# Performance work log

Measured on AMD Instinct MI355X. Metric: run time of the kernel, lower is better.

The kernel has to match this reference:

```python
import jax, jax.numpy as jnp
import numpy as np

N = 20000
E = 320000
IN_C, HID, OUT_C = 128, 64, 32
H12, H3 = 4, 1  # heads for conv1/conv2 and conv3
NEG_SLOPE = 0.2


def _glorot(key, shape):
    fan_in, fan_out = shape[0], shape[-1]
    lim = (6.0 / (fan_in + fan_out)) ** 0.5
    return jax.random.uniform(key, shape, jnp.float32, -lim, lim)


def setup_inputs() -> dict:
    key = jax.random.key(0)
    ks = jax.random.split(key, 16)
    x = jax.random.normal(ks[0], (N, IN_C), jnp.float32)
    edge_index = jax.random.randint(ks[1], (2, E), 0, N, jnp.int64)
    p = {
        'W1': _glorot(ks[2], (IN_C, H12 * HID)),
        'as1': _glorot(ks[3], (H12, HID)), 'ad1': _glorot(ks[4], (H12, HID)),
        'b1': jnp.zeros((HID,), jnp.float32),
        'W2': _glorot(ks[5], (HID, H12 * HID)),
        'as2': _glorot(ks[6], (H12, HID)), 'ad2': _glorot(ks[7], (H12, HID)),
        'b2': jnp.zeros((HID,), jnp.float32),
        'W3': _glorot(ks[8], (HID, H3 * OUT_C)),
        'as3': _glorot(ks[9], (H3, OUT_C)), 'ad3': _glorot(ks[10], (H3, OUT_C)),
        'b3': jnp.zeros((OUT_C,), jnp.float32),
        'Wm': _glorot(ks[11], (OUT_C, OUT_C)), 'bm': jnp.zeros((OUT_C,), jnp.float32),
        'Wv': _glorot(ks[12], (OUT_C, OUT_C)), 'bv': jnp.zeros((OUT_C,), jnp.float32),
    }
    return dict(x=x, edge_index=edge_index, **p)


def gat_layer(x, src, dst, W, a_src, a_dst, b, heads, out_c):
    # x: [N, in_c] -> h: [N, H, C]
    h = (x @ W).reshape(-1, heads, out_c)
    alpha_s = jnp.einsum('nhc,hc->nh', h, a_src)  # [N,H]
    alpha_d = jnp.einsum('nhc,hc->nh', h, a_dst)
    e = jax.nn.leaky_relu(alpha_s[src] + alpha_d[dst], NEG_SLOPE)  # [E',H]
    # segment softmax over incoming edges of each dst node
    m = jax.ops.segment_max(e, dst, num_segments=N)
    p = jnp.exp(e - m[dst])
    s = jax.ops.segment_sum(p, dst, num_segments=N)
    alpha = p / (s[dst] + 1e-16)  # [E',H]
    msg = h[src] * alpha[:, :, None]  # [E',H,C]
    out = jax.ops.segment_sum(msg, dst, num_segments=N)  # [N,H,C]
    return out.mean(axis=1) + b  # concat=False -> mean over heads


def reference(x, edge_index, W1, as1, ad1, b1, W2, as2, ad2, b2,
              W3, as3, ad3, b3, Wm, bm, Wv, bv):
    # PyG GATConv default: add self loops
    loop = jnp.arange(N, dtype=edge_index.dtype)
    src = jnp.concatenate([edge_index[0], loop])
    dst = jnp.concatenate([edge_index[1], loop])

    h = jax.nn.relu(gat_layer(x, src, dst, W1, as1, ad1, b1, H12, HID))
    h = jax.nn.relu(gat_layer(h, src, dst, W2, as2, ad2, b2, H12, HID))
    z = gat_layer(h, src, dst, W3, as3, ad3, b3, H3, OUT_C)

    z_mean = z @ Wm + bm
    z_var = jnp.clip(jnp.exp(z @ Wv + bv), 1e-8, 100.0)
    return (z_mean, z_var, z)
```

## Files before the change

kernel.cpp:

```cpp
#include <hip/hip_runtime.h>
#include <hip/hip_bf16.h>

typedef unsigned short ushortT;
typedef short short8 __attribute__((ext_vector_type(8)));
typedef unsigned short ushort8v __attribute__((ext_vector_type(8)));
typedef float float4v __attribute__((ext_vector_type(4)));

constexpr int Nn   = 20000;
constexpr int Ee   = 320000;
constexpr int EP   = Ee + Nn;
constexpr float NSL = 0.2f;
constexpr int CAP  = 128;

__device__ __forceinline__ float b2f(__hip_bfloat16 v) { return __bfloat162float(v); }
__device__ __forceinline__ float bits2f(unsigned short u) {
    __hip_bfloat16 b; *(unsigned short*)&b = u; return __bfloat162float(b);
}
__device__ __forceinline__ unsigned short f2bits(float v) {
    __hip_bfloat16 b = __float2bfloat16(v); return *(unsigned short*)&b;
}
__device__ __forceinline__ float ldf(const void* p, size_t i, int bf) {
    return bf ? __bfloat162float(((const __hip_bfloat16*)p)[i])
              : ((const float*)p)[i];
}
__device__ __forceinline__ void stf(void* p, size_t i, float v, int bf) {
    if (bf) ((__hip_bfloat16*)p)[i] = __float2bfloat16(v);
    else    ((float*)p)[i] = v;
}

__global__ void probe_k(const int* __restrict__ ei, const unsigned* __restrict__ xbits,
                        int* __restrict__ eflag, int* __restrict__ fflag,
                        int* __restrict__ cnt) {
    int gi = blockIdx.x * 256 + threadIdx.x;
    if (gi < Nn) cnt[gi] = 0;
    if (blockIdx.x != 0) return;
    __shared__ int bad, c_s;
    if (threadIdx.x == 0) { bad = 0; c_s = 0; }
    __syncthreads();
    for (int i = threadIdx.x; i < 1024; i += 256)
        if (ei[2 * i + 1] != 0) bad = 1;
    int c = 0;
    for (int i = threadIdx.x; i < 512; i += 256) {
        unsigned e = (xbits[i] >> 7) & 0xFFu;
        if (e >= 110u && e <= 135u) ++c;
    }
    atomicAdd(&c_s, c);
    __syncthreads();
    if (threadIdx.x == 0) {
        *eflag = bad ? 0 : 1;
        *fflag = (c_s > 384) ? 1 : 0;
    }
}

__device__ __forceinline__ void load_edge(const int* __restrict__ ei, int sh, int e,
                                          int& si, int& di) {
    if (e < Ee) {
        si = ei[(size_t)e << sh];
        di = ei[(size_t)(Ee + e) << sh];
    } else {
        si = di = e - Ee;
    }
}

__global__ void prep_k(const void* __restrict__ W1, const void* __restrict__ W2,
                       ushortT* __restrict__ WT1, ushortT* __restrict__ WT2,
                       const int* __restrict__ fflag) {
    const int bf = *fflag;
    int idx = blockIdx.x * 256 + threadIdx.x;
    if (idx < 256 * 128) {
        int j = idx >> 7, k = idx & 127;
        WT1[idx] = f2bits(ldf(W1, (size_t)k * 256 + j, bf));
    } else {
        int i2 = idx - 256 * 128;
        if (i2 < 256 * 64) {
            int j = i2 >> 6, k = i2 & 63;
            WT2[i2] = f2bits(ldf(W2, (size_t)k * 256 + j, bf));
        }
    }
}

__global__ void scatter_k(const int* __restrict__ ei, const int* __restrict__ eflag,
                          int* __restrict__ cnt, int* __restrict__ csr) {
    int e = blockIdx.x * 256 + threadIdx.x;
    if (e >= EP) return;
    int sh = *eflag, si, di;
    load_edge(ei, sh, e, si, di);
    int pos = atomicAdd(cnt + di, 1);
    if (pos < CAP) csr[di * CAP + pos] = si;
}

template <int XMODE, int INC>
__global__ __launch_bounds__(256) void gemm_mfma(const void* __restrict__ xg,
                                                 const ushortT* __restrict__ WT,
                                                 ushortT* __restrict__ h,
                                                 const void* __restrict__ avs,
                                                 const void* __restrict__ avd,
                                                 float* __restrict__ as_, float* __restrict__ ad_,
                                                 const int* __restrict__ fflag) {
    constexpr int SW = INC + 8, SX = INC + 8, CPR = INC / 8;
    const int bf  = *fflag;
    const int xbf = (XMODE == 0) ? bf : 1;
    __shared__ ushortT wt_s[128 * SW];
    __shared__ ushortT xs[64 * SX];
    const int base = blockIdx.x * 64;
    const int jh   = blockIdx.y;
    const ushortT* WTg = WT + (size_t)jh * 128 * INC;
    for (int ch = threadIdx.x; ch < 128 * CPR; ch += 256) {
        int j = ch / CPR, kc = (ch - j * CPR) * 8;
        *(short8*)(wt_s + j * SW + kc) = *(const short8*)(WTg + j * INC + kc);
    }
    for (int ch = threadIdx.x; ch < 64 * CPR; ch += 256) {
        int nl = ch / CPR, kc = (ch - nl * CPR) * 8;
        int node = base + nl;
        short8 v = {0, 0, 0, 0, 0, 0, 0, 0};
        if (node < Nn) {
            if (xbf) {
                v = *(const short8*)((const ushortT*)xg + (size_t)node * INC + kc);
            } else {
                const float* xf = (const float*)xg + (size_t)node * INC + kc;
#pragma unroll
                for (int i = 0; i < 8; ++i) v[i] = (short)f2bits(xf[i]);
            }
        }
        *(short8*)(xs + nl * SX + kc) = v;
    }
    __syncthreads();
    const int lane = threadIdx.x & 63, w = threadIdx.x >> 6;
    const int ln = lane & 15, quad = lane >> 4;
    float4v acc[8];
#pragma unroll
    for (int T = 0; T < 8; ++T) acc[T] = (float4v){0.f, 0.f, 0.f, 0.f};
#pragma unroll
    for (int ks = 0; ks < INC / 32; ++ks) {
        const int kb = ks * 32 + quad * 8;
        const short8 b = *(const short8*)(xs + (w * 16 + ln) * SX + kb);
#pragma unroll
        for (int T = 0; T < 8; ++T) {
            const short8 a = *(const short8*)(wt_s + (T * 16 + ln) * SW + kb);
            acc[T] = __builtin_amdgcn_mfma_f32_16x16x32_bf16(a, b, acc[T], 0, 0, 0);
        }
    }
    const int node = base + w * 16 + ln;
    const bool live = (node < Nn);
    ushortT* hn = h + (size_t)node * 256;
    float pas0 = 0, pas1 = 0, pad0 = 0, pad1 = 0;
#pragma unroll
    for (int T = 0; T < 8; ++T) {
        const int jb = jh * 128 + T * 16 + quad * 4;
#pragma unroll
        for (int r = 0; r < 4; ++r) {
            const int j = jb + r;
            const float v = acc[T][r];
            if (live) hn[(j & 63) * 4 + (j >> 6)] = f2bits(v);
            const float was = ldf(avs, j, bf), wad = ldf(avd, j, bf);
            if (T < 4) { pas0 = fmaf(v, was, pas0); pad0 = fmaf(v, wad, pad0); }
            else       { pas1 = fmaf(v, was, pas1); pad1 = fmaf(v, wad, pad1); }
        }
    }
#pragma unroll
    for (int off = 16; off < 64; off <<= 1) {
        pas0 += __shfl_xor(pas0, off, 64);
        pas1 += __shfl_xor(pas1, off, 64);
        pad0 += __shfl_xor(pad0, off, 64);
        pad1 += __shfl_xor(pad1, off, 64);
    }
    if (lane < 16 && live) {
        as_[node * 4 + jh * 2]     = pas0;
        as_[node * 4 + jh * 2 + 1] = pas1;
        ad_[node * 4 + jh * 2]     = pad0;
        ad_[node * 4 + jh * 2 + 1] = pad1;
    }
}

__global__ __launch_bounds__(256) void gemm_small(const float* __restrict__ x,
                                                  const void* __restrict__ W,
                                                  __hip_bfloat16* __restrict__ h,
                                                  const void* __restrict__ avs,
                                                  const void* __restrict__ avd,
                                                  float* __restrict__ as_, float* __restrict__ ad_,
                                                  const int* __restrict__ fflag, int N) {
    constexpr int INC = 64, R = 32, PAD = R + 4;
    const int bf = *fflag;
    __shared__ float xsh[INC * PAD];
    int base = blockIdx.x * R;
    for (int i = threadIdx.x; i < R * INC; i += 256) {
        int rr = i / INC, kk = i - rr * INC;
        int nn = base + rr;
        xsh[kk * PAD + rr] = (nn < N) ? x[(size_t)nn * INC + kk] : 0.0f;
    }
    __syncthreads();
    const int jc = threadIdx.x & 31;
    const int g  = threadIdx.x >> 5;
    float acc[4] = {};
    if (bf) {
        const __hip_bfloat16* Wb = (const __hip_bfloat16*)W;
#pragma unroll 4
        for (int k = 0; k < INC; ++k) {
            float4 xv = *(const float4*)(xsh + k * PAD + g * 4);
            float w = b2f(Wb[k * 32 + jc]);
            acc[0] = fmaf(xv.x, w, acc[0]);
            acc[1] = fmaf(xv.y, w, acc[1]);
            acc[2] = fmaf(xv.z, w, acc[2]);
            acc[3] = fmaf(xv.w, w, acc[3]);
        }
    } else {
        const float* Wf = (const float*)W;
#pragma unroll 4
        for (int k = 0; k < INC; ++k) {
            float4 xv = *(const float4*)(xsh + k * PAD + g * 4);
            float w = Wf[k * 32 + jc];
            acc[0] = fmaf(xv.x, w, acc[0]);
            acc[1] = fmaf(xv.y, w, acc[1]);
            acc[2] = fmaf(xv.z, w, acc[2]);
            acc[3] = fmaf(xv.w, w, acc[3]);
        }
    }
    float avsr = ldf(avs, jc, bf), avdr = ldf(avd, jc, bf);
#pragma unroll
    for (int m = 0; m < 4; ++m) {
        int n = base + g * 4 + m;
        if (n >= N) continue;
        h[(size_t)n * 32 + jc] = __float2bfloat16(acc[m]);
        float t1 = acc[m] * avsr;
        float t2 = acc[m] * avdr;
#pragma unroll
        for (int off = 16; off > 0; off >>= 1) {
            t1 += __shfl_down(t1, off, 32);
            t2 += __shfl_down(t2, off, 32);
        }
        if (jc == 0) { as_[n] = t1; ad_[n] = t2; }
    }
}

__device__ __forceinline__ void agg_pair2(int idx, bool valid, int src0, int src1,
                                          const float* __restrict__ lal_row,
                                          const ushortT* __restrict__ h, int cl, float* a) {
    int sa = __shfl(src0, idx & 63, 64);
    int sb = __shfl(src1, idx & 63, 64);
    int src = (idx < 64) ? sa : sb;
    int off = valid ? src * 256 : 0;
    float4 ev = valid ? *(const float4*)(lal_row + idx * 4) : make_float4(0.f, 0.f, 0.f, 0.f);
    ushort8v hv = *(const ushort8v*)(h + off + cl * 8);
    a[0] = fmaf(ev.x, bits2f(hv[0]), a[0]);
    a[1] = fmaf(ev.y, bits2f(hv[1]), a[1]);
    a[2] = fmaf(ev.z, bits2f(hv[2]), a[2]);
    a[3] = fmaf(ev.w, bits2f(hv[3]), a[3]);
    a[4] = fmaf(ev.x, bits2f(hv[4]), a[4]);
    a[5] = fmaf(ev.y, bits2f(hv[5]), a[5]);
    a[6] = fmaf(ev.z, bits2f(hv[6]), a[6]);
    a[7] = fmaf(ev.w, bits2f(hv[7]), a[7]);
}

template <bool RELU>
__global__ __launch_bounds__(256) void aggr4_k(const int* __restrict__ cnt,
                                               const int* __restrict__ csr,
                                               const float* __restrict__ as_,
                                               const float* __restrict__ ad_,
                                               const unsigned short* __restrict__ h,
                                               const void* __restrict__ bias,
                                               const int* __restrict__ fflag,
                                               float* __restrict__ outF,
                                               ushortT* __restrict__ outB, int N) {
    __shared__ float lal[4][CAP][4];
    const int lane = threadIdx.x & 63, seg = threadIdx.x >> 6;
    int d = blockIdx.x * 4 + seg;
    if (d >= N) return;
    const int deg = min(cnt[d], CAP);
    const int base = d * CAP;
    const float4 adv = *(const float4*)(ad_ + d * 4);
    const int src0 = (lane < deg) ? csr[base + lane] : 0;
    const int src1 = (64 + lane < deg) ? csr[base + 64 + lane] : 0;
    float s0 = 0, s1 = 0, s2 = 0, s3 = 0;
    if (lane < deg) {
        float4 av = *(const float4*)(as_ + src0 * 4);
        float v0 = av.x + adv.x; v0 = v0 > 0.f ? v0 : NSL * v0; float e0 = __expf(v0);
        float v1 = av.y + adv.y; v1 = v1 > 0.f ? v1 : NSL * v1; float e1 = __expf(v1);
        float v2 = av.z + adv.z; v2 = v2 > 0.f ? v2 : NSL * v2; float e2 = __expf(v2);
        float v3 = av.w + adv.w; v3 = v3 > 0.f ? v3 : NSL * v3; float e3 = __expf(v3);
        s0 += e0; s1 += e1; s2 += e2; s3 += e3;
        *(float4*)(&lal[seg][lane][0]) = make_float4(e0, e1, e2, e3);
    }
    if (64 + lane < deg) {
        float4 av = *(const float4*)(as_ + src1 * 4);
        float v0 = av.x + adv.x; v0 = v0 > 0.f ? v0 : NSL * v0; float e0 = __expf(v0);
        float v1 = av.y + adv.y; v1 = v1 > 0.f ? v1 : NSL * v1; float e1 = __expf(v1);
        float v2 = av.z + adv.z; v2 = v2 > 0.f ? v2 : NSL * v2; float e2 = __expf(v2);
        float v3 = av.w + adv.w; v3 = v3 > 0.f ? v3 : NSL * v3; float e3 = __expf(v3);
        s0 += e0; s1 += e1; s2 += e2; s3 += e3;
        *(float4*)(&lal[seg][64 + lane][0]) = make_float4(e0, e1, e2, e3);
    }
    const int hl = lane >> 5, cl = lane & 31;
    const float* lal_s = &lal[seg][0][0];
    float a[8] = {0, 0, 0, 0, 0, 0, 0, 0};
    int e = 0;
    for (; e + 8 <= deg; e += 8) {
        agg_pair2(e + hl,     true, src0, src1, lal_s, h, cl, a);
        agg_pair2(e + 2 + hl, true, src0, src1, lal_s, h, cl, a);
        agg_pair2(e + 4 + hl, true, src0, src1, lal_s, h, cl, a);
        agg_pair2(e + 6 + hl, true, src0, src1, lal_s, h, cl, a);
    }
    for (; e < deg; e += 2)
        agg_pair2(e + hl, (e + hl) < deg, src0, src1, lal_s, h, cl, a);
#pragma unroll
    for (int off = 1; off < 64; off <<= 1) {
        s0 += __shfl_xor(s0, off, 64);
        s1 += __shfl_xor(s1, off, 64);
        s2 += __shfl_xor(s2, off, 64);
        s3 += __shfl_xor(s3, off, 64);
    }
    const float i0 = 0.25f / (s0 + 1e-16f), i1 = 0.25f / (s1 + 1e-16f);
    const float i2 = 0.25f / (s2 + 1e-16f), i3 = 0.25f / (s3 + 1e-16f);
#pragma unroll
    for (int i = 0; i < 8; ++i) a[i] += __shfl_xor(a[i], 32, 64);
    if (hl == 0) {
        const int bf = *fflag;
        float r0 = i0 * a[0] + i1 * a[1] + i2 * a[2] + i3 * a[3] + ldf(bias, 2 * cl, bf);
        float r1 = i0 * a[4] + i1 * a[5] + i2 * a[6] + i3 * a[7] + ldf(bias, 2 * cl + 1, bf);
        if (RELU) { r0 = fmaxf(r0, 0.f); r1 = fmaxf(r1, 0.f); }
        if (outF) *(float2*)(outF + (size_t)d * 64 + 2 * cl) = make_float2(r0, r1);
        if (outB) {
            ushort2 p; p.x = f2bits(r0); p.y = f2bits(r1);
            *(ushort2*)(outB + (size_t)d * 64 + 2 * cl) = p;
        }
    }
}

__global__ __launch_bounds__(256) void aggr1f_k(const int* __restrict__ cnt,
                                                const int* __restrict__ csr,
                                                const float* __restrict__ as_,
                                                const float* __restrict__ ad_,
                                                const __hip_bfloat16* __restrict__ h,
                                                const void* __restrict__ b3,
                                                const void* __restrict__ Wm,
                                                const void* __restrict__ bm,
                                                const void* __restrict__ Wv,
                                                const void* __restrict__ bv,
                                                const int* __restrict__ fflag,
                                                void* __restrict__ out, int N) {
    __shared__ float wm_s[1024], wv_s[1024];
    __shared__ float lal[8][CAP];
    __shared__ int   lof[8][CAP];
    const int bf = *fflag;
    for (int i = threadIdx.x; i < 1024; i += 256) {
        wm_s[i] = ldf(Wm, i, bf);
        wv_s[i] = ldf(Wv, i, bf);
    }
    __syncthreads();
    const int c = threadIdx.x & 31, seg = threadIdx.x >> 5;
    const int d = blockIdx.x * 8 + seg;
    if (d >= N) return;
    const int deg = min(cnt[d], CAP);
    const int base = d * CAP;
    const float advd = ad_[d];
    float s = 0;
    for (int i = c; i < deg; i += 32) {
        int src = csr[base + i];
        float v = as_[src] + advd;
        v = v > 0.f ? v : NSL * v;
        float ev = __expf(v);
        s += ev;
        lal[seg][i] = ev;
        lof[seg][i] = src * 32;
    }
    float acc = 0.0f;
    int e = 0;
    for (; e + 4 <= deg; e += 4) {
        float ev0 = lal[seg][e], ev1 = lal[seg][e + 1];
        float ev2 = lal[seg][e + 2], ev3 = lal[seg][e + 3];
        int o0 = lof[seg][e], o1 = lof[seg][e + 1];
        int o2 = lof[seg][e + 2], o3 = lof[seg][e + 3];
        float h0 = b2f(h[o0 + c]), h1 = b2f(h[o1 + c]);
        float h2 = b2f(h[o2 + c]), h3 = b2f(h[o3 + c]);
        acc = fmaf(ev0, h0, acc);
        acc = fmaf(ev1, h1, acc);
        acc = fmaf(ev2, h2, acc);
        acc = fmaf(ev3, h3, acc);
    }
    for (; e < deg; ++e) acc = fmaf(lal[seg][e], b2f(h[lof[seg][e] + c]), acc);
#pragma unroll
    for (int off = 1; off < 32; off <<= 1) s += __shfl_xor(s, off, 32);
    const float inv = 1.0f / (s + 1e-16f);
    const float z = inv * acc + ldf(b3, c, bf);
    stf(out, (size_t)2 * N * 32 + (size_t)d * 32 + c, z, bf);
    float sm = ldf(bm, c, bf), sv = ldf(bv, c, bf);
#pragma unroll 8
    for (int k = 0; k < 32; ++k) {
        float zk = __shfl(z, k, 32);
        sm = fmaf(zk, wm_s[k * 32 + c], sm);
        sv = fmaf(zk, wv_s[k * 32 + c], sv);
    }
    float var = __expf(sv);
    var = fminf(fmaxf(var, 1e-8f), 100.0f);
    stf(out, (size_t)d * 32 + c, sm, bf);
    stf(out, (size_t)N * 32 + (size_t)d * 32 + c, var, bf);
}

extern "C" void kernel_launch(void* const* d_in, const int* in_sizes, int n_in,
                              void* d_out, int out_size, void* d_ws, size_t ws_size,
                              hipStream_t stream) {
    const void* x   = d_in[0];
    const int*  ei  = (const int*)d_in[1];
    const void* W1  = d_in[2];
    const void* as1 = d_in[3];
    const void* ad1 = d_in[4];
    const void* b1  = d_in[5];
    const void* W2  = d_in[6];
    const void* as2 = d_in[7];
    const void* ad2 = d_in[8];
    const void* b2  = d_in[9];
    const void* W3  = d_in[10];
    const void* as3 = d_in[11];
    const void* ad3 = d_in[12];
    const void* b3  = d_in[13];
    const void* Wm  = d_in[14];
    const void* bm  = d_in[15];
    const void* Wv  = d_in[16];
    const void* bv  = d_in[17];

    float* ws = (float*)d_ws;
    ushortT* h    = (ushortT*)ws;
    ushortT* x1b  = (ushortT*)(ws + 2560000);
    float*  x2    = ws + 3200000;
    float*  as_   = ws + 4480000;
    float*  ad_   = ws + 4560000;
    ushortT* WT1  = (ushortT*)(ws + 4640000);
    ushortT* WT2  = (ushortT*)(ws + 4656384);
    int*    cnt   = (int*)(ws + 4664576);
    int*    csr   = (int*)(ws + 4684576);
    int*    eflag = (int*)(ws + 7244576);
    int*    fflag = (int*)(ws + 7244577);

    probe_k<<<79, 256, 0, stream>>>(ei, (const unsigned*)x, eflag, fflag, cnt);
    prep_k<<<192, 256, 0, stream>>>(W1, W2, WT1, WT2, fflag);
    scatter_k<<<(EP + 255) / 256, 256, 0, stream>>>(ei, eflag, cnt, csr);

    dim3 gg(313, 2);
    gemm_mfma<0, 128><<<gg, 256, 0, stream>>>(x, WT1, h, as1, ad1, as_, ad_, fflag);
    aggr4_k<true><<<5000, 256, 0, stream>>>(cnt, csr, as_, ad_, h, b1, fflag,
                                            nullptr, x1b, Nn);

    gemm_mfma<1, 64><<<gg, 256, 0, stream>>>(x1b, WT2, h, as2, ad2, as_, ad_, fflag);
    aggr4_k<true><<<5000, 256, 0, stream>>>(cnt, csr, as_, ad_, h, b2, fflag,
                                            x2, nullptr, Nn);

    gemm_small<<<625, 256, 0, stream>>>(x2, W3, (__hip_bfloat16*)h, as3, ad3, as_, ad_, fflag, Nn);
    aggr1f_k<<<2500, 256, 0, stream>>>(cnt, csr, as_, ad_, (const __hip_bfloat16*)h,
                                       b3, Wm, bm, Wv, bv, fflag, d_out, Nn);
}
```

Before: 237.0 us.

## Switch h to head-major layout and compute edge weights inline in aggregation

The GEMM now stores h in head-major order (head*64+channel), so each thread writes packed ushort4 values instead of scattered single elements. It also stages the attention vectors in shared memory. Both aggregation kernels drop the LDS staging of exp-weights and source offsets and instead compute each edge's weight redundantly per lane while gathering. Each lane now covers one head and 8 channels, with cross-lane shuffles reducing over heads at the end. This removes the LDS round trip and a barrier-like phase, at the cost of redundant exp and as_ loads per lane.

```diff
diff --git a/kernel.cpp b/kernel.cpp
--- a/kernel.cpp
+++ b/kernel.cpp
@@ -102,6 +102,7 @@
     const int xbf = (XMODE == 0) ? bf : 1;
     __shared__ ushortT wt_s[128 * SW];
     __shared__ ushortT xs[64 * SX];
+    __shared__ float av_s[2][128];
     const int base = blockIdx.x * 64;
     const int jh   = blockIdx.y;
     const ushortT* WTg = WT + (size_t)jh * 128 * INC;
@@ -124,6 +125,10 @@
         }
         *(short8*)(xs + nl * SX + kc) = v;
     }
+    if (threadIdx.x < 128) {
+        av_s[0][threadIdx.x] = ldf(avs, jh * 128 + threadIdx.x, bf);
+        av_s[1][threadIdx.x] = ldf(avd, jh * 128 + threadIdx.x, bf);
+    }
     __syncthreads();
     const int lane = threadIdx.x & 63, w = threadIdx.x >> 6;
     const int ln = lane & 15, quad = lane >> 4;
@@ -142,17 +147,19 @@
     }
     const int node = base + w * 16 + ln;
     const bool live = (node < Nn);
-    ushortT* hn = h + (size_t)node * 256;
+    ushortT* hn = h + (size_t)node * 256 + jh * 128;
     float pas0 = 0, pas1 = 0, pad0 = 0, pad1 = 0;
 #pragma unroll
     for (int T = 0; T < 8; ++T) {
-        const int jb = jh * 128 + T * 16 + quad * 4;
+        const int jl = T * 16 + quad * 4;
+        ushort4 pk;
+        pk.x = f2bits(acc[T][0]); pk.y = f2bits(acc[T][1]);
+        pk.z = f2bits(acc[T][2]); pk.w = f2bits(acc[T][3]);
+        if (live) *(ushort4*)(hn + jl) = pk;
 #pragma unroll
         for (int r = 0; r < 4; ++r) {
-            const int j = jb + r;
             const float v = acc[T][r];
-            if (live) hn[(j & 63) * 4 + (j >> 6)] = f2bits(v);
-            const float was = ldf(avs, j, bf), wad = ldf(avd, j, bf);
+            const float was = av_s[0][jl + r], wad = av_s[1][jl + r];
             if (T < 4) { pas0 = fmaf(v, was, pas0); pad0 = fmaf(v, wad, pad0); }
             else       { pas1 = fmaf(v, was, pas1); pad1 = fmaf(v, wad, pad1); }
         }
@@ -232,25 +239,6 @@
     }
 }
 
-__device__ __forceinline__ void agg_pair2(int idx, bool valid, int src0, int src1,
-                                          const float* __restrict__ lal_row,
-                                          const ushortT* __restrict__ h, int cl, float* a) {
-    int sa = __shfl(src0, idx & 63, 64);
-    int sb = __shfl(src1, idx & 63, 64);
-    int src = (idx < 64) ? sa : sb;
-    int off = valid ? src * 256 : 0;
-    float4 ev = valid ? *(const float4*)(lal_row + idx * 4) : make_float4(0.f, 0.f, 0.f, 0.f);
-    ushort8v hv = *(const ushort8v*)(h + off + cl * 8);
-    a[0] = fmaf(ev.x, bits2f(hv[0]), a[0]);
-    a[1] = fmaf(ev.y, bits2f(hv[1]), a[1]);
-    a[2] = fmaf(ev.z, bits2f(hv[2]), a[2]);
-    a[3] = fmaf(ev.w, bits2f(hv[3]), a[3]);
-    a[4] = fmaf(ev.x, bits2f(hv[4]), a[4]);
-    a[5] = fmaf(ev.y, bits2f(hv[5]), a[5]);
-    a[6] = fmaf(ev.z, bits2f(hv[6]), a[6]);
-    a[7] = fmaf(ev.w, bits2f(hv[7]), a[7]);
-}
-
 template <bool RELU>
 __global__ __launch_bounds__(256) void aggr4_k(const int* __restrict__ cnt,
                                                const int* __restrict__ csr,
@@ -261,66 +249,71 @@
                                                const int* __restrict__ fflag,
                                                float* __restrict__ outF,
                                                ushortT* __restrict__ outB, int N) {
-    __shared__ float lal[4][CAP][4];
     const int lane = threadIdx.x & 63, seg = threadIdx.x >> 6;
     int d = blockIdx.x * 4 + seg;
     if (d >= N) return;
     const int deg = min(cnt[d], CAP);
     const int base = d * CAP;
     const float4 adv = *(const float4*)(ad_ + d * 4);
-    const int src0 = (lane < deg) ? csr[base + lane] : 0;
-    const int src1 = (64 + lane < deg) ? csr[base + 64 + lane] : 0;
+    const int hl = lane >> 5, cl = lane & 31;
+    const int q = cl >> 3, c8 = (cl & 7) * 8;
+    float a[8] = {0, 0, 0, 0, 0, 0, 0, 0};
     float s0 = 0, s1 = 0, s2 = 0, s3 = 0;
-    if (lane < deg) {
-        float4 av = *(const float4*)(as_ + src0 * 4);
+
+    auto do_edge = [&](int idx) {
+        int src = csr[base + idx];
+        float4 av = *(const float4*)(as_ + src * 4);
         float v0 = av.x + adv.x; v0 = v0 > 0.f ? v0 : NSL * v0; float e0 = __expf(v0);
         float v1 = av.y + adv.y; v1 = v1 > 0.f ? v1 : NSL * v1; float e1 = __expf(v1);
         float v2 = av.z + adv.z; v2 = v2 > 0.f ? v2 : NSL * v2; float e2 = __expf(v2);
         float v3 = av.w + adv.w; v3 = v3 > 0.f ? v3 : NSL * v3; float e3 = __expf(v3);
         s0 += e0; s1 += e1; s2 += e2; s3 += e3;
-        *(float4*)(&lal[seg][lane][0]) = make_float4(e0, e1, e2, e3);
-    }
-    if (64 + lane < deg) {
-        float4 av = *(const float4*)(as_ + src1 * 4);
-        float v0 = av.x + adv.x; v0 = v0 > 0.f ? v0 : NSL * v0; float e0 = __expf(v0);
-        float v1 = av.y + adv.y; v1 = v1 > 0.f ? v1 : NSL * v1; float e1 = __expf(v1);
-        float v2 = av.z + adv.z; v2 = v2 > 0.f ? v2 : NSL * v2; float e2 = __expf(v2);
-        float v3 = av.w + adv.w; v3 = v3 > 0.f ? v3 : NSL * v3; float e3 = __expf(v3);
-        s0 += e0; s1 += e1; s2 += e2; s3 += e3;
-        *(float4*)(&lal[seg][64 + lane][0]) = make_float4(e0, e1, e2, e3);
-    }
-    const int hl = lane >> 5, cl = lane & 31;
-    const float* lal_s = &lal[seg][0][0];
-    float a[8] = {0, 0, 0, 0, 0, 0, 0, 0};
+        float ev = (q == 0) ? e0 : (q == 1) ? e1 : (q == 2) ? e2 : e3;
+        ushort8v hv = *(const ushort8v*)(h + (size_t)src * 256 + q * 64 + c8);
+#pragma unroll
+        for (int i = 0; i < 8; ++i) a[i] = fmaf(ev, bits2f(hv[i]), a[i]);
+    };
+
     int e = 0;
     for (; e + 8 <= deg; e += 8) {
-        agg_pair2(e + hl,     true, src0, src1, lal_s, h, cl, a);
-        agg_pair2(e + 2 + hl, true, src0, src1, lal_s, h, cl, a);
-        agg_pair2(e + 4 + hl, true, src0, src1, lal_s, h, cl, a);
-        agg_pair2(e + 6 + hl, true, src0, src1, lal_s, h, cl, a);
-    }
-    for (; e < deg; e += 2)
-        agg_pair2(e + hl, (e + hl) < deg, src0, src1, lal_s, h, cl, a);
-#pragma unroll
-    for (int off = 1; off < 64; off <<= 1) {
-        s0 += __shfl_xor(s0, off, 64);
-        s1 += __shfl_xor(s1, off, 64);
-        s2 += __shfl_xor(s2, off, 64);
-        s3 += __shfl_xor(s3, off, 64);
-    }
-    const float i0 = 0.25f / (s0 + 1e-16f), i1 = 0.25f / (s1 + 1e-16f);
-    const float i2 = 0.25f / (s2 + 1e-16f), i3 = 0.25f / (s3 + 1e-16f);
-#pragma unroll
-    for (int i = 0; i < 8; ++i) a[i] += __shfl_xor(a[i], 32, 64);
-    if (hl == 0) {
+        do_edge(e + hl);
+        do_edge(e + 2 + hl);
+        do_edge(e + 4 + hl);
+        do_edge(e + 6 + hl);
+    }
+    for (; e + 2 <= deg; e += 2) do_edge(e + hl);
+    if (e < deg && hl == 0) do_edge(e);
+
+    s0 += __shfl_xor(s0, 32, 64);
+    s1 += __shfl_xor(s1, 32, 64);
+    s2 += __shfl_xor(s2, 32, 64);
+    s3 += __shfl_xor(s3, 32, 64);
+    const float sq = (q == 0) ? s0 : (q == 1) ? s1 : (q == 2) ? s2 : s3;
+    const float iq = 0.25f / (sq + 1e-16f);
+#pragma unroll
+    for (int i = 0; i < 8; ++i) {
+        a[i] *= iq;
+        a[i] += __shfl_xor(a[i], 32, 64);
+        a[i] += __shfl_xor(a[i], 8, 64);
+        a[i] += __shfl_xor(a[i], 16, 64);
+    }
+    if (lane < 8) {
         const int bf = *fflag;
-        float r0 = i0 * a[0] + i1 * a[1] + i2 * a[2] + i3 * a[3] + ldf(bias, 2 * cl, bf);
-        float r1 = i0 * a[4] + i1 * a[5] + i2 * a[6] + i3 * a[7] + ldf(bias, 2 * cl + 1, bf);
-        if (RELU) { r0 = fmaxf(r0, 0.f); r1 = fmaxf(r1, 0.f); }
-        if (outF) *(float2*)(outF + (size_t)d * 64 + 2 * cl) = make_float2(r0, r1);
+        float r[8];
+#pragma unroll
+        for (int i = 0; i < 8; ++i) {
+            r[i] = a[i] + ldf(bias, lane * 8 + i, bf);
+            if (RELU) r[i] = fmaxf(r[i], 0.f);
+        }
+        if (outF) {
+            *(float4*)(outF + (size_t)d * 64 + lane * 8)     = make_float4(r[0], r[1], r[2], r[3]);
+            *(float4*)(outF + (size_t)d * 64 + lane * 8 + 4) = make_float4(r[4], r[5], r[6], r[7]);
+        }
         if (outB) {
-            ushort2 p; p.x = f2bits(r0); p.y = f2bits(r1);
-            *(ushort2*)(outB + (size_t)d * 64 + 2 * cl) = p;
+            ushort8v p;
+#pragma unroll
+            for (int i = 0; i < 8; ++i) p[i] = f2bits(r[i]);
+            *(ushort8v*)(outB + (size_t)d * 64 + lane * 8) = p;
         }
     }
 }
@@ -338,8 +331,6 @@
                                                 const int* __restrict__ fflag,
                                                 void* __restrict__ out, int N) {
     __shared__ float wm_s[1024], wv_s[1024];
-    __shared__ float lal[8][CAP];
-    __shared__ int   lof[8][CAP];
     const int bf = *fflag;
     for (int i = threadIdx.x; i < 1024; i += 256) {
         wm_s[i] = ldf(Wm, i, bf);
@@ -352,33 +343,22 @@
     const int deg = min(cnt[d], CAP);
     const int base = d * CAP;
     const float advd = ad_[d];
-    float s = 0;
-    for (int i = c; i < deg; i += 32) {
-        int src = csr[base + i];
+    float s = 0, acc = 0;
+
+    auto do_edge1 = [&](int idx) {
+        int src = csr[base + idx];
         float v = as_[src] + advd;
         v = v > 0.f ? v : NSL * v;
         float ev = __expf(v);
         s += ev;
-        lal[seg][i] = ev;
-        lof[seg][i] = src * 32;
-    }
-    float acc = 0.0f;
+        acc = fmaf(ev, b2f(h[src * 32 + c]), acc);
+    };
     int e = 0;
     for (; e + 4 <= deg; e += 4) {
-        float ev0 = lal[seg][e], ev1 = lal[seg][e + 1];
-        float ev2 = lal[seg][e + 2], ev3 = lal[seg][e + 3];
-        int o0 = lof[seg][e], o1 = lof[seg][e + 1];
-        int o2 = lof[seg][e + 2], o3 = lof[seg][e + 3];
-        float h0 = b2f(h[o0 + c]), h1 = b2f(h[o1 + c]);
-        float h2 = b2f(h[o2 + c]), h3 = b2f(h[o3 + c]);
-        acc = fmaf(ev0, h0, acc);
-        acc = fmaf(ev1, h1, acc);
-        acc = fmaf(ev2, h2, acc);
-        acc = fmaf(ev3, h3, acc);
-    }
-    for (; e < deg; ++e) acc = fmaf(lal[seg][e], b2f(h[lof[seg][e] + c]), acc);
-#pragma unroll
-    for (int off = 1; off < 32; off <<= 1) s += __shfl_xor(s, off, 32);
+        do_edge1(e); do_edge1(e + 1); do_edge1(e + 2); do_edge1(e + 3);
+    }
+    for (; e < deg; ++e) do_edge1(e);
+
     const float inv = 1.0f / (s + 1e-16f);
     const float z = inv * acc + ldf(b3, c, bf);
     stf(out, (size_t)2 * N * 32 + (size_t)d * 32 + c, z, bf);
```

After: 254.8 us. 1.07x slower.
